# Performance work log

Measured on AMD Instinct MI355X. Metric: run time of the kernel, lower is better.

## Reference

```python
import jax, jax.numpy as jnp
import numpy as np

D = 64          # in_out_dim
HID = 512       # hidden_dim of hypernet
WIDTH = 64      # width
BATCH = 524288
BLOCK = WIDTH * D


def setup_inputs() -> dict:
    key = jax.random.key(0)
    ks = jax.random.split(key, 9)
    def glorot(k, shape):
        fan_in, fan_out = shape
        lim = np.sqrt(6.0 / (fan_in + fan_out)).astype(np.float32)
        return jax.random.uniform(k, shape, jnp.float32, -lim, lim)
    t = jax.random.uniform(ks[0], (1,), jnp.float32)
    z = jax.random.normal(ks[1], (BATCH, D), jnp.float32)
    logp_z = jnp.zeros((BATCH, 1), jnp.float32)
    W1 = glorot(ks[2], (1, HID));    b1 = jax.random.uniform(ks[3], (HID,), jnp.float32, -1.0, 1.0)
    W2 = glorot(ks[4], (HID, HID));  b2 = jax.random.uniform(ks[5], (HID,), jnp.float32, -0.06, 0.06)
    W3 = glorot(ks[6], (HID, 3 * BLOCK + WIDTH))
    b3 = jax.random.uniform(ks[7], (3 * BLOCK + WIDTH,), jnp.float32, -0.06, 0.06)
    return {"t": t, "z": z, "logp_z": logp_z,
            "W1": W1, "b1": b1, "W2": W2, "b2": b2, "W3": W3, "b3": b3}


def reference(t, z, logp_z, W1, b1, W2, b2, W3, b3):
    # Hypernetwork: scalar t -> per-time params
    p = jnp.tanh(t.reshape(1, 1) @ W1 + b1)
    p = jnp.tanh(p @ W2 + b2)
    p = (p @ W3 + b3).reshape(-1)
    W = p[:BLOCK].reshape(WIDTH, D)                    # (w, d)
    U = p[BLOCK:2 * BLOCK].reshape(WIDTH, D)           # (w, d)
    G = p[2 * BLOCK:3 * BLOCK].reshape(WIDTH, D)
    U = U * jax.nn.sigmoid(G)
    B = p[3 * BLOCK:].reshape(WIDTH)                   # (w,)
    # h[b,w] = tanh(sum_d z[b,d] W[w,d] + B[w])
    h = jnp.tanh(z @ W.T + B)                          # (batch, width)
    dz_dt = (h @ U) / WIDTH                            # mean over width -> (batch, d)
    # Exact Jacobian trace: tr(df/dz)[b] = mean_w (1 - h[b,w]^2) * sum_d W[w,d] U[w,d]
    wu = jnp.sum(W * U, axis=1)                        # (width,)
    trace = ((1.0 - h * h) @ wu) / WIDTH               # (batch,)
    dlogp_z_dt = -trace[:, None]                       # (batch, 1)
    return dz_dt, dlogp_z_dt
```

## Files before the change

### kernel.cpp

```cpp
#include <hip/hip_runtime.h>
#include <hip/hip_bf16.h>

#define HID 512
#define NW 64
#define BATCH 524288
#define BLK 4096
#define P3N 12352
#define KSPLIT 8

typedef __attribute__((ext_vector_type(8))) short short8;
typedef __attribute__((ext_vector_type(4))) float f32x4;

__device__ __forceinline__ unsigned short f2bf(float f){
  unsigned u = __float_as_uint(f);
  unsigned r = u + 0x7fffu + ((u >> 16) & 1u);
  return (unsigned short)(r >> 16);
}
__device__ __forceinline__ float bf2f(unsigned short s){
  return __uint_as_float(((unsigned)s) << 16);
}
__device__ __forceinline__ float fast_tanh(float x){
  float e = __expf(2.0f * x);
  return 1.0f - 2.0f * __builtin_amdgcn_rcpf(e + 1.0f);
}

__global__ __launch_bounds__(256) void k_hyper12(
    const float* __restrict__ t, const float* __restrict__ W1, const float* __restrict__ b1,
    const float* __restrict__ W2, const float* __restrict__ b2, float* __restrict__ p2)
{
  __shared__ float sp1[HID];
  int tid = threadIdx.x;
  float tv = t[0];
  for (int i = tid; i < HID; i += 256)
    sp1[i] = tanhf(tv * W1[i] + b1[i]);
  __syncthreads();
  int n = blockIdx.x * 8 + (tid >> 5);
  int sub = tid & 31;
  float acc = 0.f;
  #pragma unroll 4
  for (int j = 0; j < HID/32; ++j){
    int k = sub + 32*j;
    acc += sp1[k] * W2[(size_t)k*HID + n];
  }
  #pragma unroll
  for (int m = 1; m < 32; m <<= 1) acc += __shfl_xor(acc, m);
  if (sub == 0) p2[n] = tanhf(acc + b2[n]);
}

__global__ __launch_bounds__(256) void k_hyper3(
    const float* __restrict__ p2, const float* __restrict__ W3, float* __restrict__ p3p)
{
  __shared__ float sp2[HID/KSPLIT];
  int tid = threadIdx.x;
  int bn = blockIdx.x % 49;
  int bk = blockIdx.x / 49;
  int k0 = bk * (HID/KSPLIT);
  if (tid < HID/KSPLIT) sp2[tid] = p2[k0 + tid];
  __syncthreads();
  int n = bn*256 + tid;
  if (n < P3N){
    float acc = 0.f;
    const float* w3 = W3 + (size_t)k0 * P3N + n;
    #pragma unroll 8
    for (int k = 0; k < HID/KSPLIT; ++k)
      acc += sp2[k] * w3[(size_t)k * P3N];
    p3p[(size_t)bk * P3N + n] = acc;
  }
}

__global__ __launch_bounds__(256) void k_params(
    const float* __restrict__ p3p, const float* __restrict__ b3,
    unsigned short* __restrict__ Wb, unsigned short* __restrict__ Utb,
    float* __restrict__ Bv, float* __restrict__ wu)
{
  __shared__ float swu[NW];
  int tid = threadIdx.x;
  if (tid < NW) swu[tid] = 0.f;
  __syncthreads();
  for (int i = tid; i < BLK; i += 256){
    float pW = b3[i], pU = b3[BLK + i], pG = b3[2*BLK + i];
    #pragma unroll
    for (int s = 0; s < KSPLIT; ++s){
      pW += p3p[(size_t)s*P3N + i];
      pU += p3p[(size_t)s*P3N + BLK + i];
      pG += p3p[(size_t)s*P3N + 2*BLK + i];
    }
    float sg = 1.0f / (1.0f + expf(-pG));
    float Uv = pU * sg;
    int w = i >> 6, d = i & 63;
    Wb[i] = f2bf(pW);
    Utb[d*NW + w] = f2bf(Uv);
    atomicAdd(&swu[w], pW * Uv);
  }
  __syncthreads();
  if (tid < NW){
    wu[tid] = swu[tid];
    float bb = b3[3*BLK + tid];
    #pragma unroll
    for (int s = 0; s < KSPLIT; ++s) bb += p3p[(size_t)s*P3N + 3*BLK + tid];
    Bv[tid] = bb;
  }
}

__global__ __launch_bounds__(256, 2) void k_main(
    const float* __restrict__ z,
    const unsigned short* __restrict__ Wb, const unsigned short* __restrict__ Utb,
    const float* __restrict__ Bv, const float* __restrict__ wu,
    float* __restrict__ dz, float* __restrict__ dlogp)
{
  __shared__ unsigned short hs[4][16][72];
  int tid = threadIdx.x;
  int wv = tid >> 6;
  int lane = tid & 63;
  int r = lane & 15;
  int g = lane >> 4;

  short8 Wf[4][2], Uf[4][2];
  #pragma unroll
  for (int n = 0; n < 4; ++n){
    #pragma unroll
    for (int kt = 0; kt < 2; ++kt){
      Wf[n][kt] = *(const short8*)(Wb  + ((n*16 + r)*64 + kt*32 + g*8));
      Uf[n][kt] = *(const short8*)(Utb + ((n*16 + r)*64 + kt*32 + g*8));
    }
  }
  float Bvl[4], wul[4];
  #pragma unroll
  for (int n = 0; n < 4; ++n){ Bvl[n] = Bv[n*16 + r]; wul[n] = wu[n*16 + r]; }

  long rowbase = (long)blockIdx.x * 128 + wv * 32;

  #pragma unroll
  for (int t = 0; t < 2; ++t){
    long tilerow = rowbase + t*16;
    short8 zh[2], zl[2];
    #pragma unroll
    for (int kt = 0; kt < 2; ++kt){
      const float* zp = z + (tilerow + r)*64 + kt*32 + g*8;
      float4 v0 = *(const float4*)(zp);
      float4 v1 = *(const float4*)(zp + 4);
      float zv[8] = {v0.x, v0.y, v0.z, v0.w, v1.x, v1.y, v1.z, v1.w};
      #pragma unroll
      for (int j = 0; j < 8; ++j){
        unsigned short h_ = f2bf(zv[j]);
        zh[kt][j] = (short)h_;
        zl[kt][j] = (short)f2bf(zv[j] - bf2f(h_));
      }
    }
    f32x4 acc1[4];
    #pragma unroll
    for (int n = 0; n < 4; ++n){ f32x4 zro = {0.f,0.f,0.f,0.f}; acc1[n] = zro; }
    #pragma unroll
    for (int kt = 0; kt < 2; ++kt){
      #pragma unroll
      for (int n = 0; n < 4; ++n){
        acc1[n] = __builtin_amdgcn_mfma_f32_16x16x32_bf16(zh[kt], Wf[n][kt], acc1[n], 0,0,0);
        acc1[n] = __builtin_amdgcn_mfma_f32_16x16x32_bf16(zl[kt], Wf[n][kt], acc1[n], 0,0,0);
      }
    }
    float tp[4] = {0.f,0.f,0.f,0.f};
    #pragma unroll
    for (int n = 0; n < 4; ++n){
      #pragma unroll
      for (int q = 0; q < 4; ++q){
        float h = fast_tanh(acc1[n][q] + Bvl[n]);
        tp[q] += (1.0f - h*h) * wul[n];
        hs[wv][g*4 + q][n*16 + r] = f2bf(h);
      }
    }
    #pragma unroll
    for (int q = 0; q < 4; ++q){
      #pragma unroll
      for (int m = 1; m < 16; m <<= 1) tp[q] += __shfl_xor(tp[q], m);
    }
    if (r == 0){
      #pragma unroll
      for (int q = 0; q < 4; ++q)
        dlogp[tilerow + g*4 + q] = -tp[q] * (1.0f/64.0f);
    }
    __syncthreads();
    short8 hf[2];
    #pragma unroll
    for (int kt = 0; kt < 2; ++kt)
      hf[kt] = *(const short8*)(&hs[wv][r][kt*32 + g*8]);
    f32x4 acc2[4];
    #pragma unroll
    for (int n = 0; n < 4; ++n){ f32x4 zro = {0.f,0.f,0.f,0.f}; acc2[n] = zro; }
    #pragma unroll
    for (int kt = 0; kt < 2; ++kt){
      #pragma unroll
      for (int n = 0; n < 4; ++n)
        acc2[n] = __builtin_amdgcn_mfma_f32_16x16x32_bf16(hf[kt], Uf[n][kt], acc2[n], 0,0,0);
    }
    #pragma unroll
    for (int n = 0; n < 4; ++n){
      #pragma unroll
      for (int q = 0; q < 4; ++q)
        dz[(tilerow + g*4 + q)*64 + n*16 + r] = acc2[n][q] * (1.0f/64.0f);
    }
    __syncthreads();
  }
}

extern "C" void kernel_launch(void* const* d_in, const int* in_sizes, int n_in,
                              void* d_out, int out_size, void* d_ws, size_t ws_size,
                              hipStream_t stream)
{
  const float* t  = (const float*)d_in[0];
  const float* z  = (const float*)d_in[1];
  const float* W1 = (const float*)d_in[3];
  const float* b1 = (const float*)d_in[4];
  const float* W2 = (const float*)d_in[5];
  const float* b2 = (const float*)d_in[6];
  const float* W3 = (const float*)d_in[7];
  const float* b3 = (const float*)d_in[8];

  float* ws   = (float*)d_ws;
  float* p2   = ws;
  float* p3p  = ws + 512;
  float* tail = ws + 512 + 8*P3N;
  unsigned short* Wb  = (unsigned short*)(tail);
  unsigned short* Utb = (unsigned short*)(tail + 2048);
  float* Bv = tail + 4096;
  float* wu = tail + 4160;

  float* dz    = (float*)d_out;
  float* dlogp = dz + (size_t)BATCH*64;

  hipLaunchKernelGGL(k_hyper12, dim3(64),        dim3(256), 0, stream, t, W1, b1, W2, b2, p2);
  hipLaunchKernelGGL(k_hyper3,  dim3(49*KSPLIT), dim3(256), 0, stream, p2, W3, p3p);
  hipLaunchKernelGGL(k_params,  dim3(1),         dim3(256), 0, stream, p3p, b3, Wb, Utb, Bv, wu);
  hipLaunchKernelGGL(k_main,    dim3(BATCH/128), dim3(256), 0, stream, z, Wb, Utb, Bv, wu, dz, dlogp);
}
```

Before: 296.9 us.

## Vectorize output stores via transposed MFMA, drop barriers, parallelize param prep

The second MFMA's operands are swapped so each lane holds four consecutive dz columns. That lets dz and dlogp be written as 16-byte nontemporal stores instead of scattered 4-byte stores. The h staging buffer in shared memory is now private to each wave and tile, so both __syncthreads barriers are removed. The z hi/lo bf16 split now uses byte-permute instructions, occupancy is raised to 4 blocks per CU, and the trace is computed as sum(wu) minus sum(h^2·wu). k_params is spread over 16 blocks and reduces wu with wave shuffles instead of shared-memory atomics. The risks are extra register pressure from the higher occupancy bound and a slightly different bf16 rounding of h.

```diff
diff --git a/kernel.cpp b/kernel.cpp
--- a/kernel.cpp
+++ b/kernel.cpp
@@ -11,17 +11,42 @@
 typedef __attribute__((ext_vector_type(8))) short short8;
 typedef __attribute__((ext_vector_type(4))) float f32x4;
 
+union V8 { short8 s; unsigned int w[4]; };
+
 __device__ __forceinline__ unsigned short f2bf(float f){
   unsigned u = __float_as_uint(f);
   unsigned r = u + 0x7fffu + ((u >> 16) & 1u);
   return (unsigned short)(r >> 16);
 }
-__device__ __forceinline__ float bf2f(unsigned short s){
-  return __uint_as_float(((unsigned)s) << 16);
-}
 __device__ __forceinline__ float fast_tanh(float x){
   float e = __expf(2.0f * x);
   return 1.0f - 2.0f * __builtin_amdgcn_rcpf(e + 1.0f);
+}
+
+__device__ __forceinline__ void split8(f32x4 a, f32x4 b, short8& hi, short8& lo){
+  unsigned u0=__float_as_uint(a[0]), u1=__float_as_uint(a[1]),
+           u2=__float_as_uint(a[2]), u3=__float_as_uint(a[3]),
+           u4=__float_as_uint(b[0]), u5=__float_as_uint(b[1]),
+           u6=__float_as_uint(b[2]), u7=__float_as_uint(b[3]);
+  V8 H;
+  H.w[0] = __builtin_amdgcn_perm(u1, u0, 0x07060302u);
+  H.w[1] = __builtin_amdgcn_perm(u3, u2, 0x07060302u);
+  H.w[2] = __builtin_amdgcn_perm(u5, u4, 0x07060302u);
+  H.w[3] = __builtin_amdgcn_perm(u7, u6, 0x07060302u);
+  float l0 = a[0] - __uint_as_float(u0 & 0xffff0000u);
+  float l1 = a[1] - __uint_as_float(u1 & 0xffff0000u);
+  float l2 = a[2] - __uint_as_float(u2 & 0xffff0000u);
+  float l3 = a[3] - __uint_as_float(u3 & 0xffff0000u);
+  float l4 = b[0] - __uint_as_float(u4 & 0xffff0000u);
+  float l5 = b[1] - __uint_as_float(u5 & 0xffff0000u);
+  float l6 = b[2] - __uint_as_float(u6 & 0xffff0000u);
+  float l7 = b[3] - __uint_as_float(u7 & 0xffff0000u);
+  V8 L;
+  L.w[0] = __builtin_amdgcn_perm(__float_as_uint(l1), __float_as_uint(l0), 0x07060302u);
+  L.w[1] = __builtin_amdgcn_perm(__float_as_uint(l3), __float_as_uint(l2), 0x07060302u);
+  L.w[2] = __builtin_amdgcn_perm(__float_as_uint(l5), __float_as_uint(l4), 0x07060302u);
+  L.w[3] = __builtin_amdgcn_perm(__float_as_uint(l7), __float_as_uint(l6), 0x07060302u);
+  hi = H.s; lo = L.s;
 }
 
 __global__ __launch_bounds__(256) void k_hyper12(
@@ -73,47 +98,41 @@
     unsigned short* __restrict__ Wb, unsigned short* __restrict__ Utb,
     float* __restrict__ Bv, float* __restrict__ wu)
 {
-  __shared__ float swu[NW];
   int tid = threadIdx.x;
-  if (tid < NW) swu[tid] = 0.f;
-  __syncthreads();
-  for (int i = tid; i < BLK; i += 256){
-    float pW = b3[i], pU = b3[BLK + i], pG = b3[2*BLK + i];
-    #pragma unroll
-    for (int s = 0; s < KSPLIT; ++s){
-      pW += p3p[(size_t)s*P3N + i];
-      pU += p3p[(size_t)s*P3N + BLK + i];
-      pG += p3p[(size_t)s*P3N + 2*BLK + i];
-    }
-    float sg = 1.0f / (1.0f + expf(-pG));
-    float Uv = pU * sg;
-    int w = i >> 6, d = i & 63;
-    Wb[i] = f2bf(pW);
-    Utb[d*NW + w] = f2bf(Uv);
-    atomicAdd(&swu[w], pW * Uv);
-  }
-  __syncthreads();
-  if (tid < NW){
-    wu[tid] = swu[tid];
-    float bb = b3[3*BLK + tid];
-    #pragma unroll
-    for (int s = 0; s < KSPLIT; ++s) bb += p3p[(size_t)s*P3N + 3*BLK + tid];
-    Bv[tid] = bb;
-  }
-}
-
-__global__ __launch_bounds__(256, 2) void k_main(
+  int i = blockIdx.x*256 + tid;
+  float pW = b3[i], pU = b3[BLK + i], pG = b3[2*BLK + i];
+  #pragma unroll
+  for (int s = 0; s < KSPLIT; ++s){
+    pW += p3p[(size_t)s*P3N + i];
+    pU += p3p[(size_t)s*P3N + BLK + i];
+    pG += p3p[(size_t)s*P3N + 2*BLK + i];
+  }
+  float Uv = pU / (1.0f + expf(-pG));
+  int w = i >> 6, d = i & 63;
+  Wb[i] = f2bf(pW);
+  Utb[d*NW + w] = f2bf(Uv);
+  float v = pW * Uv;
+  #pragma unroll
+  for (int m = 1; m < 64; m <<= 1) v += __shfl_xor(v, m);
+  if ((tid & 63) == 0) wu[w] = v;
+  if (blockIdx.x == 0 && tid < NW){
+    float pB = b3[3*BLK + tid];
+    #pragma unroll
+    for (int s = 0; s < KSPLIT; ++s) pB += p3p[(size_t)s*P3N + 3*BLK + tid];
+    Bv[tid] = pB;
+  }
+}
+
+__global__ __launch_bounds__(256, 4) void k_main(
     const float* __restrict__ z,
     const unsigned short* __restrict__ Wb, const unsigned short* __restrict__ Utb,
     const float* __restrict__ Bv, const float* __restrict__ wu,
     float* __restrict__ dz, float* __restrict__ dlogp)
 {
-  __shared__ unsigned short hs[4][16][72];
-  int tid = threadIdx.x;
-  int wv = tid >> 6;
-  int lane = tid & 63;
-  int r = lane & 15;
-  int g = lane >> 4;
+  __shared__ unsigned short hs[4][2][16][72];
+  const int tid = threadIdx.x;
+  const int wv = tid >> 6, lane = tid & 63;
+  const int r = lane & 15, g = lane >> 4;
 
   short8 Wf[4][2], Uf[4][2];
   #pragma unroll
@@ -127,78 +146,76 @@
   float Bvl[4], wul[4];
   #pragma unroll
   for (int n = 0; n < 4; ++n){ Bvl[n] = Bv[n*16 + r]; wul[n] = wu[n*16 + r]; }
-
-  long rowbase = (long)blockIdx.x * 128 + wv * 32;
+  const float swul = wul[0] + wul[1] + wul[2] + wul[3];
+
+  const long rowbase = (long)blockIdx.x * 128 + wv * 32;
 
   #pragma unroll
   for (int t = 0; t < 2; ++t){
-    long tilerow = rowbase + t*16;
-    short8 zh[2], zl[2];
-    #pragma unroll
-    for (int kt = 0; kt < 2; ++kt){
-      const float* zp = z + (tilerow + r)*64 + kt*32 + g*8;
-      float4 v0 = *(const float4*)(zp);
-      float4 v1 = *(const float4*)(zp + 4);
-      float zv[8] = {v0.x, v0.y, v0.z, v0.w, v1.x, v1.y, v1.z, v1.w};
-      #pragma unroll
-      for (int j = 0; j < 8; ++j){
-        unsigned short h_ = f2bf(zv[j]);
-        zh[kt][j] = (short)h_;
-        zl[kt][j] = (short)f2bf(zv[j] - bf2f(h_));
-      }
-    }
+    const long tr_ = rowbase + t*16;
+    const float* zp = z + (tr_ + r)*64 + g*8;
+    f32x4 za0 = *(const f32x4*)(zp);
+    f32x4 za1 = *(const f32x4*)(zp + 4);
+    f32x4 zb0 = *(const f32x4*)(zp + 32);
+    f32x4 zb1 = *(const f32x4*)(zp + 36);
+
+    short8 zh0, zl0, zh1, zl1;
+    split8(za0, za1, zh0, zl0);
+    split8(zb0, zb1, zh1, zl1);
+
     f32x4 acc1[4];
     #pragma unroll
     for (int n = 0; n < 4; ++n){ f32x4 zro = {0.f,0.f,0.f,0.f}; acc1[n] = zro; }
     #pragma unroll
-    for (int kt = 0; kt < 2; ++kt){
-      #pragma unroll
-      for (int n = 0; n < 4; ++n){
-        acc1[n] = __builtin_amdgcn_mfma_f32_16x16x32_bf16(zh[kt], Wf[n][kt], acc1[n], 0,0,0);
-        acc1[n] = __builtin_amdgcn_mfma_f32_16x16x32_bf16(zl[kt], Wf[n][kt], acc1[n], 0,0,0);
-      }
-    }
+    for (int n = 0; n < 4; ++n){
+      acc1[n] = __builtin_amdgcn_mfma_f32_16x16x32_bf16(zh0, Wf[n][0], acc1[n], 0,0,0);
+      acc1[n] = __builtin_amdgcn_mfma_f32_16x16x32_bf16(zh1, Wf[n][1], acc1[n], 0,0,0);
+      acc1[n] = __builtin_amdgcn_mfma_f32_16x16x32_bf16(zl0, Wf[n][0], acc1[n], 0,0,0);
+      acc1[n] = __builtin_amdgcn_mfma_f32_16x16x32_bf16(zl1, Wf[n][1], acc1[n], 0,0,0);
+    }
+
     float tp[4] = {0.f,0.f,0.f,0.f};
     #pragma unroll
     for (int n = 0; n < 4; ++n){
       #pragma unroll
       for (int q = 0; q < 4; ++q){
         float h = fast_tanh(acc1[n][q] + Bvl[n]);
-        tp[q] += (1.0f - h*h) * wul[n];
-        hs[wv][g*4 + q][n*16 + r] = f2bf(h);
+        tp[q] = fmaf(-h*h, wul[n], tp[q]);
+        hs[wv][t][g*4 + q][n*16 + r] =
+            (unsigned short)((__float_as_uint(h) + 0x8000u) >> 16);
       }
     }
+
+    short8 hf0 = *(const short8*)(&hs[wv][t][r][g*8]);
+    short8 hf1 = *(const short8*)(&hs[wv][t][r][32 + g*8]);
+
+    f32x4 acc2[4];
+    #pragma unroll
+    for (int n = 0; n < 4; ++n){ f32x4 zro = {0.f,0.f,0.f,0.f}; acc2[n] = zro; }
+    #pragma unroll
+    for (int n = 0; n < 4; ++n){
+      acc2[n] = __builtin_amdgcn_mfma_f32_16x16x32_bf16(Uf[n][0], hf0, acc2[n], 0,0,0);
+      acc2[n] = __builtin_amdgcn_mfma_f32_16x16x32_bf16(Uf[n][1], hf1, acc2[n], 0,0,0);
+    }
+    #pragma unroll
+    for (int n = 0; n < 4; ++n){
+      f32x4 o = acc2[n] * 0.015625f;
+      __builtin_nontemporal_store(o, (f32x4*)(dz + (tr_ + r)*64 + n*16 + g*4));
+    }
+
     #pragma unroll
     for (int q = 0; q < 4; ++q){
-      #pragma unroll
-      for (int m = 1; m < 16; m <<= 1) tp[q] += __shfl_xor(tp[q], m);
+      tp[q] += swul;
+      tp[q] += __shfl_xor(tp[q], 1);
+      tp[q] += __shfl_xor(tp[q], 2);
+      tp[q] += __shfl_xor(tp[q], 4);
+      tp[q] += __shfl_xor(tp[q], 8);
     }
     if (r == 0){
-      #pragma unroll
-      for (int q = 0; q < 4; ++q)
-        dlogp[tilerow + g*4 + q] = -tp[q] * (1.0f/64.0f);
-    }
-    __syncthreads();
-    short8 hf[2];
-    #pragma unroll
-    for (int kt = 0; kt < 2; ++kt)
-      hf[kt] = *(const short8*)(&hs[wv][r][kt*32 + g*8]);
-    f32x4 acc2[4];
-    #pragma unroll
-    for (int n = 0; n < 4; ++n){ f32x4 zro = {0.f,0.f,0.f,0.f}; acc2[n] = zro; }
-    #pragma unroll
-    for (int kt = 0; kt < 2; ++kt){
-      #pragma unroll
-      for (int n = 0; n < 4; ++n)
-        acc2[n] = __builtin_amdgcn_mfma_f32_16x16x32_bf16(hf[kt], Uf[n][kt], acc2[n], 0,0,0);
-    }
-    #pragma unroll
-    for (int n = 0; n < 4; ++n){
-      #pragma unroll
-      for (int q = 0; q < 4; ++q)
-        dz[(tilerow + g*4 + q)*64 + n*16 + r] = acc2[n][q] * (1.0f/64.0f);
-    }
-    __syncthreads();
+      f32x4 o = { -tp[0]*0.015625f, -tp[1]*0.015625f,
+                  -tp[2]*0.015625f, -tp[3]*0.015625f };
+      __builtin_nontemporal_store(o, (f32x4*)(dlogp + tr_ + g*4));
+    }
   }
 }
 
@@ -229,6 +246,6 @@
 
   hipLaunchKernelGGL(k_hyper12, dim3(64),        dim3(256), 0, stream, t, W1, b1, W2, b2, p2);
   hipLaunchKernelGGL(k_hyper3,  dim3(49*KSPLIT), dim3(256), 0, stream, p2, W3, p3p);
-  hipLaunchKernelGGL(k_params,  dim3(1),         dim3(256), 0, stream, p3p, b3, Wb, Utb, Bv, wu);
+  hipLaunchKernelGGL(k_params,  dim3(16),        dim3(256), 0, stream, p3p, b3, Wb, Utb, Bv, wu);
   hipLaunchKernelGGL(k_main,    dim3(BATCH/128), dim3(256), 0, stream, z, Wb, Utb, Bv, wu, dz, dlogp);
 }
```

After: 295.1 us. About the same (-0.6%).
